# Kernel optimization log

Measured on AMD Instinct MI355X. Metric: run time of the kernel, lower is better.

Reference implementation:

```python
import jax, jax.numpy as jnp
import numpy as np

GRID = 64
DX = 1.0 / GRID            # grid spacing (buffer dx)
RADIUS = 2.5 * DX          # search_radius = dx * 2.5
CIN, COUT = 16, 16
B, N = 2, 8192
EPS = 1e-12
FOUR_OVER_PI = 4.0 / np.pi


def _safe_sqrt(v):
    return jnp.sqrt(jnp.maximum(v, EPS))


def _sphere_to_cylinder(x, y, z):
    # volume-preserving map: unit ball -> cylinder (radius 1, height 2)
    sq = x * x + y * y + z * z
    norm = _safe_sqrt(sq)
    xy2 = x * x + y * y
    cap = 1.25 * z * z > xy2                      # polar-cap region
    s_cap = jnp.sqrt(3.0 * norm / (norm + jnp.abs(z) + EPS))
    s_side = norm / _safe_sqrt(xy2)
    xc = jnp.where(cap, x * s_cap, x * s_side)
    yc = jnp.where(cap, y * s_cap, y * s_side)
    zc = jnp.where(cap, jnp.sign(z) * norm, 1.5 * z)
    zero = sq <= EPS
    z0 = jnp.zeros_like(x)
    return (jnp.where(zero, z0, xc), jnp.where(zero, z0, yc), jnp.where(zero, z0, zc))


def _cylinder_to_cube(x, y, z):
    # area-preserving disc -> square on the xy cross-section
    xy2 = x * x + y * y
    nxy = _safe_sqrt(xy2)
    xdom = jnp.abs(y) <= jnp.abs(x)
    safe_x = jnp.where(jnp.abs(x) > EPS, x, 1.0)
    safe_y = jnp.where(jnp.abs(y) > EPS, y, 1.0)
    tx = jnp.sign(x) * nxy
    ty = jnp.sign(y) * nxy
    xa, ya = tx, tx * FOUR_OVER_PI * jnp.arctan(y / safe_x)
    xb, yb = ty * FOUR_OVER_PI * jnp.arctan(x / safe_y), ty
    xc = jnp.where(xdom, xa, xb)
    yc = jnp.where(xdom, ya, yb)
    zero = xy2 <= EPS
    z0 = jnp.zeros_like(x)
    return jnp.where(zero, z0, xc), jnp.where(zero, z0, yc), z


def _cconv_forward(input, pos, weights, grid_pos):
    Bb, C, D, H, Wd = input.shape
    Np = pos.shape[1]
    # [B,C,D,H,W] -> [B,D,H,W,C] -> [B,G,C]  (matches permute+view in torch)
    feat = jnp.transpose(input, (0, 2, 3, 4, 1)).reshape(Bb, D * H * Wd, C)
    # fixed 6^3 stencil of candidate grid cells around each point
    off = jnp.arange(6) - 2
    o0, o1, o2 = jnp.meshgrid(off, off, off, indexing='ij')
    offs = jnp.stack([o0, o1, o2], axis=-1).reshape(-1, 3)          # [216,3]
    base = jnp.floor(pos / DX).astype(jnp.int32)                    # [B,N,3]
    cand = base[:, :, None, :] + offs[None, None]                   # [B,N,216,3]
    dims = jnp.array([D, H, Wd])
    in_bounds = jnp.all((cand >= 0) & (cand < dims), axis=-1)       # [B,N,216]
    cc = jnp.clip(cand, 0, dims - 1)
    flat = (cc[..., 0] * H + cc[..., 1]) * Wd + cc[..., 2]          # [B,N,216]
    bidx = jnp.arange(Bb)[:, None, None]
    npos = grid_pos[flat]                                           # [B,N,216,3]
    fg = feat[bidx, flat]                                           # [B,N,216,C]
    rel = npos - pos[:, :, None, :]
    dist2 = jnp.sum(rel * rel, axis=-1)
    valid = in_bounds & (dist2 <= RADIUS * RADIUS)
    # map relative offsets (scaled to the unit ball) to the unit cube
    u = rel / RADIUS
    x, y, z = _sphere_to_cylinder(u[..., 0], u[..., 1], u[..., 2])
    x, y, z = _cylinder_to_cube(x, y, z)
    # linear interpolation of the 3x3x3 kernel, align_corners=True -> coords in [0,2]
    taps = jnp.arange(3, dtype=pos.dtype)
    def hat(c):
        c = jnp.clip((c * 0.5 + 0.5) * 2.0, 0.0, 2.0)
        return jnp.maximum(0.0, 1.0 - jnp.abs(c[..., None] - taps))  # [B,N,216,3]
    w0, w1, w2 = hat(x), hat(y), hat(z)
    w27 = jnp.einsum('bnki,bnkj,bnkl->bnkijl', w0, w1, w2).reshape(Bb, Np, -1, 27)
    w27 = w27 * valid[..., None].astype(w27.dtype)
    # accumulate interpolated features per kernel tap, then apply the kernel
    acc = jnp.einsum('bnkt,bnkc->bntc', w27, fg)                    # [B,N,27,C]
    out = jnp.einsum('bntc,tcd->bnd', acc, weights.reshape(27, C, -1))
    # normalize=True (Open3D default): divide by neighbor count
    count = jnp.sum(valid, axis=-1).astype(out.dtype)
    out = out / jnp.maximum(count, 1.0)[..., None]
    return out


def setup_inputs() -> dict:
    key = jax.random.key(0)
    k1, k2, k3 = jax.random.split(key, 3)
    inp = jax.random.normal(k1, (B, CIN, GRID, GRID, GRID), jnp.float32)
    pos = jax.random.uniform(k2, (B, N, 3), jnp.float32)
    weights = jax.random.normal(k3, (3, 3, 3, CIN, COUT), jnp.float32) * 0.05
    ax = jnp.arange(GRID, dtype=jnp.float32) * DX
    g = jnp.stack(jnp.meshgrid(ax, ax, ax, indexing='ij'), axis=-1).reshape(-1, 3)
    return {"input": inp, "pos": pos, "weights": weights, "grid_pos": g}


def reference(input, pos, weights, grid_pos):
    return _cconv_forward(input, pos, weights, grid_pos)
```

## Files before the change

kernel.cpp:

```cpp
#include <hip/hip_runtime.h>
#include <cstdint>

typedef float v2f __attribute__((ext_vector_type(2)));

namespace {
constexpr int kG = 262144;
constexpr int kB = 2;
constexpr int kN = 8192;
constexpr int kPts = kB * kN;
constexpr float kDX = 1.0f / 64.0f;
constexpr float kRad2 = 0.00152587890625f;
constexpr float kInvRad = 25.6f;
constexpr float kEps = 1e-12f;
constexpr float kFourOverPi = 1.27323954473516268615f;

constexpr int PPB = 4;
constexpr int THREADS = PPB * 64;
constexpr int MAXREC = 96;
constexpr int SLOT = 12;
constexpr int NFLAT = 96;
constexpr int GSTRIDE = MAXREC * SLOT + NFLAT;
}

__device__ __forceinline__ float sgnf(float v) {
    return (v > 0.f) ? 1.f : ((v < 0.f) ? -1.f : 0.f);
}

__global__ __launch_bounds__(256) void transpose_feat_k(const float* __restrict__ in,
                                                        float* __restrict__ feat) {
    int idx = blockIdx.x * 256 + threadIdx.x;
    if (idx >= kB * kG) return;
    int b = idx >> 18;
    int g = idx & (kG - 1);
    float v[16];
#pragma unroll
    for (int c = 0; c < 16; ++c) v[c] = in[((size_t)(b * 16 + c)) * kG + g];
    float4* dst = reinterpret_cast<float4*>(feat + (size_t)idx * 16);
    dst[0] = make_float4(v[0], v[1], v[2], v[3]);
    dst[1] = make_float4(v[4], v[5], v[6], v[7]);
    dst[2] = make_float4(v[8], v[9], v[10], v[11]);
    dst[3] = make_float4(v[12], v[13], v[14], v[15]);
}

__global__ __launch_bounds__(THREADS) void cconv_main(
    const float* __restrict__ input, const float* __restrict__ pos,
    const float* __restrict__ W, const float* __restrict__ feat,
    float* __restrict__ out, int use_feat)
{
    __shared__ __align__(16) float rec[PPB * GSTRIDE];

    const int tid = threadIdx.x;
    const int wv = tid >> 6;
    const int lane = tid & 63;
    const int sg = lane >> 4;
    const int lig = lane & 15;
    const int pt = blockIdx.x * PPB + wv;
    const int b = pt >> 13;

    const float px = pos[pt * 3 + 0];
    const float py = pos[pt * 3 + 1];
    const float pz = pos[pt * 3 + 2];
    const int bx = (int)floorf(px * 64.f);
    const int by = (int)floorf(py * 64.f);
    const int bz = (int)floorf(pz * 64.f);

    float* grec = rec + wv * GSTRIDE;
    int* iflats = reinterpret_cast<int*>(grec + MAXREC * SLOT);
    int nv = 0;

#pragma unroll
    for (int it = 0; it < 4; ++it) {
        int k = it * 64 + lane;
        bool valid = false;
        float rx = 0.f, ry = 0.f, rz = 0.f;
        int flat16 = 0;
        if (k < 216) {
            int a = k / 36;
            int r = k - a * 36;
            int b1 = r / 6;
            int c1 = r - b1 * 6;
            int g0 = bx + a - 2, g1 = by + b1 - 2, g2 = bz + c1 - 2;
            bool inb = (g0 >= 0) & (g0 < 64) & (g1 >= 0) & (g1 < 64) &
                       (g2 >= 0) & (g2 < 64);
            int q0 = min(max(g0, 0), 63);
            int q1 = min(max(g1, 0), 63);
            int q2 = min(max(g2, 0), 63);
            flat16 = ((q0 * 64 + q1) * 64 + q2) << 4;
            rx = __fsub_rn((float)q0 * kDX, px);
            ry = __fsub_rn((float)q1 * kDX, py);
            rz = __fsub_rn((float)q2 * kDX, pz);
            float d2 = __fadd_rn(__fadd_rn(__fmul_rn(rx, rx), __fmul_rn(ry, ry)),
                                 __fmul_rn(rz, rz));
            valid = inb && (d2 <= kRad2);
        }
        unsigned long long ball = __ballot(valid);
        if (valid) {
            int slot = nv + __popcll(ball & ((1ull << lane) - 1ull));
            *reinterpret_cast<float4*>(grec + slot * SLOT) =
                make_float4(rx, ry, rz, 0.f);
            iflats[slot] = flat16;
        }
        nv += (int)__popcll(ball);
    }
    __builtin_amdgcn_wave_barrier();

    for (int z = nv + lane; z < MAXREC; z += 64) {
        float4 zf = make_float4(0.f, 0.f, 0.f, 0.f);
        float4* zp = reinterpret_cast<float4*>(grec + z * SLOT);
        zp[0] = zf; zp[1] = zf; zp[2] = zf;
        iflats[z] = 0;
    }
    __builtin_amdgcn_wave_barrier();

    const float* fbp = use_feat ? (feat + (size_t)b * kG * 16)
                                : (input + (size_t)b * 16 * kG);
#define LDF(IDX) (use_feat ? fbp[(size_t)iflats[(IDX)] + lig]                 \
                           : fbp[(size_t)lig * kG + (iflats[(IDX)] >> 4)])
    float fa0 = LDF(sg),      fa1 = LDF(sg + 4);
    float fa2 = LDF(sg + 8),  fa3 = LDF(sg + 12);
    float fb0 = LDF(sg + 16), fb1 = LDF(sg + 20);
    float fb2 = LDF(sg + 24), fb3 = LDF(sg + 28);

    for (int s = lane; s < nv; s += 64) {
        float* rp = grec + s * SLOT;
        float4 rc = *reinterpret_cast<const float4*>(rp);
        float ux = rc.x * kInvRad, uy = rc.y * kInvRad, uz = rc.z * kInvRad;

        float xx = ux * ux, yy = uy * uy, zz = uz * uz;
        float xy2 = xx + yy;
        float sq = xy2 + zz;
        float nrm = __builtin_amdgcn_sqrtf(fmaxf(sq, kEps));
        bool cap = (1.25f * zz > xy2);
        float scap = __builtin_amdgcn_sqrtf(3.f * nrm) *
                     __builtin_amdgcn_rsqf(nrm + fabsf(uz) + kEps);
        float sside = nrm * __builtin_amdgcn_rsqf(fmaxf(xy2, kEps));
        float sc = cap ? scap : sside;
        float xc = ux * sc, yc = uy * sc;
        float zc = cap ? sgnf(uz) * nrm : 1.5f * uz;
        if (sq <= kEps) { xc = 0.f; yc = 0.f; zc = 0.f; }

        float xy2b = xc * xc + yc * yc;
        float nxy = __builtin_amdgcn_sqrtf(fmaxf(xy2b, kEps));
        bool xdom = (fabsf(yc) <= fabsf(xc));
        float num = xdom ? yc : xc;
        float den = xdom ? xc : yc;
        float dsafe = (fabsf(den) > kEps) ? den : 1.0f;
        float r = num * __builtin_amdgcn_rcpf(dsafe);
        float r2 = r * r;
        float at = -0.01172120f;
        at = at * r2 + 0.05265332f;
        at = at * r2 - 0.11643287f;
        at = at * r2 + 0.19354346f;
        at = at * r2 - 0.33262347f;
        at = at * r2 + 0.99997726f;
        at = at * r;
        float tt = sgnf(den) * nxy;
        float g = tt * kFourOverPi * at;
        float xo = xdom ? tt : g;
        float yo = xdom ? g : tt;
        if (xy2b <= kEps) { xo = 0.f; yo = 0.f; }
        float zo = zc;

        float tx = fminf(fmaxf(xo + 1.f, 0.f), 2.f) - 1.f;
        float ty = fminf(fmaxf(yo + 1.f, 0.f), 2.f) - 1.f;
        float tz = fminf(fmaxf(zo + 1.f, 0.f), 2.f) - 1.f;
        float wx0 = fmaxf(0.f, -tx), wx1 = 1.f - fabsf(tx), wx2 = fmaxf(0.f, tx);
        float wy0 = fmaxf(0.f, -ty), wy1 = 1.f - fabsf(ty), wy2 = fmaxf(0.f, ty);
        float wz0 = fmaxf(0.f, -tz), wz1 = 1.f - fabsf(tz);

        float4* rp4 = reinterpret_cast<float4*>(rp);
        rp4[0] = make_float4(wx0 * wy0, wx0 * wy1, wx0 * wy2, wx1 * wy0);
        rp4[1] = make_float4(wx1 * wy1, wx1 * wy2, wx2 * wy0, wx2 * wy1);
        rp4[2] = make_float4(wx2 * wy2, wz0, wz1, 0.f);
    }
    __builtin_amdgcn_wave_barrier();

    v2f az0_01 = {0.f, 0.f}, az1_01 = {0.f, 0.f}, az2_01 = {0.f, 0.f};
    v2f az0_23 = {0.f, 0.f}, az1_23 = {0.f, 0.f}, az2_23 = {0.f, 0.f};
    v2f az0_45 = {0.f, 0.f}, az1_45 = {0.f, 0.f}, az2_45 = {0.f, 0.f};
    v2f az0_67 = {0.f, 0.f}, az1_67 = {0.f, 0.f}, az2_67 = {0.f, 0.f};
    float a8_0 = 0.f, a8_1 = 0.f, a8_2 = 0.f;

    const int nvp16 = (nv + 15) & ~15;
    const int M = nvp16 >> 4;

#define REC_FMA(S, FV)                                                        \
  {                                                                           \
    const float4* rp4_ = reinterpret_cast<const float4*>(grec + (S) * SLOT);  \
    float4 Wa = rp4_[0], Wb = rp4_[1], Wc = rp4_[2];                          \
    float m0 = Wc.y * (FV), m1 = Wc.z * (FV);                                 \
    float m2 = ((1.f - Wc.y) - Wc.z) * (FV);                                  \
    v2f mz0 = {m0, m0}, mz1 = {m1, m1}, mz2 = {m2, m2};                       \
    v2f p01 = {Wa.x, Wa.y}, p23 = {Wa.z, Wa.w};                               \
    v2f p45 = {Wb.x, Wb.y}, p67 = {Wb.z, Wb.w};                               \
    az0_01 = __builtin_elementwise_fma(p01, mz0, az0_01);                     \
    az1_01 = __builtin_elementwise_fma(p01, mz1, az1_01);                     \
    az2_01 = __builtin_elementwise_fma(p01, mz2, az2_01);                     \
    az0_23 = __builtin_elementwise_fma(p23, mz0, az0_23);                     \
    az1_23 = __builtin_elementwise_fma(p23, mz1, az1_23);                     \
    az2_23 = __builtin_elementwise_fma(p23, mz2, az2_23);                     \
    az0_45 = __builtin_elementwise_fma(p45, mz0, az0_45);                     \
    az1_45 = __builtin_elementwise_fma(p45, mz1, az1_45);                     \
    az2_45 = __builtin_elementwise_fma(p45, mz2, az2_45);                     \
    az0_67 = __builtin_elementwise_fma(p67, mz0, az0_67);                     \
    az1_67 = __builtin_elementwise_fma(p67, mz1, az1_67);                     \
    az2_67 = __builtin_elementwise_fma(p67, mz2, az2_67);                     \
    a8_0 = __builtin_fmaf(Wc.x, m0, a8_0);                                    \
    a8_1 = __builtin_fmaf(Wc.x, m1, a8_1);                                    \
    a8_2 = __builtin_fmaf(Wc.x, m2, a8_2);                                    \
  }

#define P2BODY(KK, F0_, F1_, F2_, F3_)                                        \
  {                                                                           \
    const int rb_ = (KK) * 16 + sg;                                           \
    float nf0_ = 0.f, nf1_ = 0.f, nf2_ = 0.f, nf3_ = 0.f;                     \
    const bool dol_ = (M > (KK) + 2);                                         \
    if (dol_) {                                                               \
      int q0_ = iflats[rb_ + 32], q1_ = iflats[rb_ + 36],                     \
          q2_ = iflats[rb_ + 40], q3_ = iflats[rb_ + 44];                     \
      if (use_feat) {                                                         \
        nf0_ = fbp[(size_t)q0_ + lig]; nf1_ = fbp[(size_t)q1_ + lig];         \
        nf2_ = fbp[(size_t)q2_ + lig]; nf3_ = fbp[(size_t)q3_ + lig];         \
      } else {                                                                \
        nf0_ = fbp[(size_t)lig * kG + (q0_ >> 4)];                            \
        nf1_ = fbp[(size_t)lig * kG + (q1_ >> 4)];                            \
        nf2_ = fbp[(size_t)lig * kG + (q2_ >> 4)];                            \
        nf3_ = fbp[(size_t)lig * kG + (q3_ >> 4)];                            \
      }                                                                       \
    }                                                                         \
    REC_FMA(rb_,      F0_); REC_FMA(rb_ + 4,  F1_);                           \
    REC_FMA(rb_ + 8,  F2_); REC_FMA(rb_ + 12, F3_);                           \
    if (dol_) { F0_ = nf0_; F1_ = nf1_; F2_ = nf2_; F3_ = nf3_; }             \
  }

    if (M > 0) P2BODY(0, fa0, fa1, fa2, fa3)
    if (M > 1) P2BODY(1, fb0, fb1, fb2, fb3)
    if (M > 2) P2BODY(2, fa0, fa1, fa2, fa3)
    if (M > 3) P2BODY(3, fb0, fb1, fb2, fb3)
    if (M > 4) P2BODY(4, fa0, fa1, fa2, fa3)
    if (M > 5) P2BODY(5, fb0, fb1, fb2, fb3)

    float acc[28] = {
        az0_01.x, az1_01.x, az2_01.x,
        az0_01.y, az1_01.y, az2_01.y,
        az0_23.x, az1_23.x, az2_23.x,
        az0_23.y, az1_23.y, az2_23.y,
        az0_45.x, az1_45.x, az2_45.x,
        az0_45.y, az1_45.y, az2_45.y,
        az0_67.x, az1_67.x, az2_67.x,
        az0_67.y, az1_67.y, az2_67.y,
        a8_0,     a8_1,     a8_2,
        0.f
    };

    const bool hi32 = (lane >= 32);
    float kp[14];
#pragma unroll
    for (int j = 0; j < 14; ++j) {
        float send = hi32 ? acc[j] : acc[14 + j];
        float recv = __shfl_xor(send, 32);
        kp[j] = (hi32 ? acc[14 + j] : acc[j]) + recv;
    }
    const bool hi16 = (lane & 16) != 0;
    float kk[7];
#pragma unroll
    for (int j = 0; j < 7; ++j) {
        float send = hi16 ? kp[j] : kp[7 + j];
        float recv = __shfl_xor(send, 16);
        kk[j] = (hi16 ? kp[7 + j] : kp[j]) + recv;
    }

    float partial[16];
#pragma unroll
    for (int d = 0; d < 16; ++d) partial[d] = 0.f;
    const float* wbase = W + (sg * 7) * 256 + lig * 16;
#pragma unroll
    for (int j = 0; j < 7; ++j) {
        if (sg * 7 + j < 27) {
            const float4* wr = reinterpret_cast<const float4*>(wbase + j * 256);
            float4 a0 = wr[0], a1 = wr[1], a2 = wr[2], a3 = wr[3];
            float at_ = kk[j];
            partial[0]  += at_ * a0.x; partial[1]  += at_ * a0.y;
            partial[2]  += at_ * a0.z; partial[3]  += at_ * a0.w;
            partial[4]  += at_ * a1.x; partial[5]  += at_ * a1.y;
            partial[6]  += at_ * a1.z; partial[7]  += at_ * a1.w;
            partial[8]  += at_ * a2.x; partial[9]  += at_ * a2.y;
            partial[10] += at_ * a2.z; partial[11] += at_ * a2.w;
            partial[12] += at_ * a3.x; partial[13] += at_ * a3.y;
            partial[14] += at_ * a3.z; partial[15] += at_ * a3.w;
        }
    }

#pragma unroll
    for (int half = 8; half >= 1; half >>= 1) {
        bool up = (lig & half) != 0;
#pragma unroll
        for (int j = 0; j < half; ++j) {
            float send = up ? partial[j] : partial[j + half];
            float recv = __shfl_xor(send, half);
            partial[j] = (up ? partial[j + half] : partial[j]) + recv;
        }
    }
    float res = partial[0];
    res += __shfl_xor(res, 16);
    res += __shfl_xor(res, 32);
    res = res / fmaxf((float)nv, 1.f);
    if (lane < 16) out[(size_t)pt * 16 + lig] = res;
#undef LDF
#undef REC_FMA
#undef P2BODY
}

extern "C" void kernel_launch(void* const* d_in, const int* in_sizes, int n_in,
                              void* d_out, int out_size, void* d_ws, size_t ws_size,
                              hipStream_t stream) {
    const float* input = (const float*)d_in[0];
    const float* pos   = (const float*)d_in[1];
    const float* W     = (const float*)d_in[2];
    float* out  = (float*)d_out;
    float* feat = (float*)d_ws;

    const size_t feat_bytes = (size_t)kB * kG * 16 * sizeof(float);
    int use_feat = (d_ws != nullptr && ws_size >= feat_bytes) ? 1 : 0;

    if (use_feat) {
        transpose_feat_k<<<(kB * kG + 255) / 256, 256, 0, stream>>>(input, feat);
    }
    cconv_main<<<kPts / PPB, THREADS, 0, stream>>>(input, pos, W, feat, out, use_feat);
}
```

Baseline: 74.84 us.

## Deepen feature prefetch to three stages, halve records granularity, shrink block

Halves points per block from 4 to 2 and adds an occupancy hint of 8 to launch_bounds. Extends the software-pipelined feature gather from two to three register buffers, so loads are issued three iterations ahead. Pads the neighbour count to a multiple of 8 rather than 16, so the trailing half-group of FMA work is skipped. The aim is to hide gather latency and cut wasted padded work, at the cost of more registers and extra branching on the tail.

```diff
diff --git a/kernel.cpp b/kernel.cpp
--- a/kernel.cpp
+++ b/kernel.cpp
@@ -14,7 +14,7 @@
 constexpr float kEps = 1e-12f;
 constexpr float kFourOverPi = 1.27323954473516268615f;
 
-constexpr int PPB = 4;
+constexpr int PPB = 2;
 constexpr int THREADS = PPB * 64;
 constexpr int MAXREC = 96;
 constexpr int SLOT = 12;
@@ -42,7 +42,7 @@
     dst[3] = make_float4(v[12], v[13], v[14], v[15]);
 }
 
-__global__ __launch_bounds__(THREADS) void cconv_main(
+__global__ __launch_bounds__(THREADS, 8) void cconv_main(
     const float* __restrict__ input, const float* __restrict__ pos,
     const float* __restrict__ W, const float* __restrict__ feat,
     float* __restrict__ out, int use_feat)
@@ -120,6 +120,8 @@
     float fa2 = LDF(sg + 8),  fa3 = LDF(sg + 12);
     float fb0 = LDF(sg + 16), fb1 = LDF(sg + 20);
     float fb2 = LDF(sg + 24), fb3 = LDF(sg + 28);
+    float fc0 = LDF(sg + 32), fc1 = LDF(sg + 36);
+    float fc2 = LDF(sg + 40), fc3 = LDF(sg + 44);
 
     for (int s = lane; s < nv; s += 64) {
         float* rp = grec + s * SLOT;
@@ -181,8 +183,9 @@
     v2f az0_67 = {0.f, 0.f}, az1_67 = {0.f, 0.f}, az2_67 = {0.f, 0.f};
     float a8_0 = 0.f, a8_1 = 0.f, a8_2 = 0.f;
 
-    const int nvp16 = (nv + 15) & ~15;
-    const int M = nvp16 >> 4;
+    const int R = (nv + 7) & ~7;
+    const int F = R >> 4;
+    const bool HB = (R & 8) != 0;
 
 #define REC_FMA(S, FV)                                                        \
   {                                                                           \
@@ -213,32 +216,23 @@
 #define P2BODY(KK, F0_, F1_, F2_, F3_)                                        \
   {                                                                           \
     const int rb_ = (KK) * 16 + sg;                                           \
-    float nf0_ = 0.f, nf1_ = 0.f, nf2_ = 0.f, nf3_ = 0.f;                     \
-    const bool dol_ = (M > (KK) + 2);                                         \
-    if (dol_) {                                                               \
-      int q0_ = iflats[rb_ + 32], q1_ = iflats[rb_ + 36],                     \
-          q2_ = iflats[rb_ + 40], q3_ = iflats[rb_ + 44];                     \
-      if (use_feat) {                                                         \
-        nf0_ = fbp[(size_t)q0_ + lig]; nf1_ = fbp[(size_t)q1_ + lig];         \
-        nf2_ = fbp[(size_t)q2_ + lig]; nf3_ = fbp[(size_t)q3_ + lig];         \
-      } else {                                                                \
-        nf0_ = fbp[(size_t)lig * kG + (q0_ >> 4)];                            \
-        nf1_ = fbp[(size_t)lig * kG + (q1_ >> 4)];                            \
-        nf2_ = fbp[(size_t)lig * kG + (q2_ >> 4)];                            \
-        nf3_ = fbp[(size_t)lig * kG + (q3_ >> 4)];                            \
-      }                                                                       \
+    const bool nxt_ = ((KK) + 3 < F) || ((KK) + 3 == F && HB);                \
+    float n0_ = 0.f, n1_ = 0.f, n2_ = 0.f, n3_ = 0.f;                         \
+    if (nxt_) {                                                               \
+      n0_ = LDF(rb_ + 48); n1_ = LDF(rb_ + 52);                               \
+      n2_ = LDF(rb_ + 56); n3_ = LDF(rb_ + 60);                               \
     }                                                                         \
-    REC_FMA(rb_,      F0_); REC_FMA(rb_ + 4,  F1_);                           \
-    REC_FMA(rb_ + 8,  F2_); REC_FMA(rb_ + 12, F3_);                           \
-    if (dol_) { F0_ = nf0_; F1_ = nf1_; F2_ = nf2_; F3_ = nf3_; }             \
+    REC_FMA(rb_, F0_); REC_FMA(rb_ + 4, F1_);                                 \
+    if ((KK) < F) { REC_FMA(rb_ + 8, F2_); REC_FMA(rb_ + 12, F3_); }          \
+    if (nxt_) { F0_ = n0_; F1_ = n1_; F2_ = n2_; F3_ = n3_; }                 \
   }
 
-    if (M > 0) P2BODY(0, fa0, fa1, fa2, fa3)
-    if (M > 1) P2BODY(1, fb0, fb1, fb2, fb3)
-    if (M > 2) P2BODY(2, fa0, fa1, fa2, fa3)
-    if (M > 3) P2BODY(3, fb0, fb1, fb2, fb3)
-    if (M > 4) P2BODY(4, fa0, fa1, fa2, fa3)
-    if (M > 5) P2BODY(5, fb0, fb1, fb2, fb3)
+     P2BODY(0, fa0, fa1, fa2, fa3)
+    if (1 < F || (1 == F && HB)) P2BODY(1, fb0, fb1, fb2, fb3)
+    if (2 < F || (2 == F && HB)) P2BODY(2, fc0, fc1, fc2, fc3)
+    if (3 < F || (3 == F && HB)) P2BODY(3, fa0, fa1, fa2, fa3)
+    if (4 < F || (4 == F && HB)) P2BODY(4, fb0, fb1, fb2, fb3)
+    if (5 == F && HB)            P2BODY(5, fc0, fc1, fc2, fc3)
 
     float acc[28] = {
         az0_01.x, az1_01.x, az2_01.x,
```

Measured after the change: 105.3 us. 1.41x slower.
